# Kernel tuning notes

Hardware: AMD Instinct MI355X
Metric: run time of the kernel (lower is better)

## Reference

```python
import jax, jax.numpy as jnp
import numpy as np

TEMP = 0.7
ALPHA_ADV = 1.0
BETA_BAND = 0.5
BAND_L = 0.05
BAND_H = 0.2
W_HEUR = 0.5
W_LEAR = 0.5


def setup_inputs() -> dict:
    key = jax.random.key(0)
    ks = jax.random.split(key, 6)
    B, Sn, C, H, W = 2, 5, 64, 192, 192
    hid = 64
    return {
        "S": jax.random.normal(ks[0], (B, C, H, W), jnp.float32),
        "T": jax.random.normal(ks[1], (B, Sn, C, H, W), jnp.float32),
        "adapt_w": jax.random.normal(ks[2], (Sn, C, C), jnp.float32) / np.sqrt(C).astype(np.float32),
        "adapt_b": jnp.zeros((Sn, C), jnp.float32),
        "r_w1": jax.random.normal(ks[3], (hid, Sn * C * 3), jnp.float32) * 0.05,
        "r_b1": jnp.zeros((hid,), jnp.float32),
        "r_w2": jax.random.normal(ks[4], (Sn, hid), jnp.float32) * 0.05,
        "r_b2": jnp.zeros((Sn,), jnp.float32),
        "ema_mu": jnp.zeros((1, Sn, C, 1, 1), jnp.float32),
        "ema_sigma": jnp.ones((1, Sn, C, 1, 1), jnp.float32),
        "ema_proxy": jnp.zeros((1, Sn, 1, 1, 1), jnp.float32),
    }


def reference(S, T, adapt_w, adapt_b, r_w1, r_b1, r_w2, r_b2, ema_mu, ema_sigma, ema_proxy):
    B, Sn, C, H, W = T.shape
    bias = adapt_b[None, :, :, None, None]
    # per-sweep 1x1 conv == per-sweep channel matmul
    T_adapt = jnp.einsum('sdc,bschw->bsdhw', adapt_w, T) + bias          # [B,S,C,H,W]
    S_rep = jnp.einsum('sdc,bchw->bsdhw', adapt_w, S) + bias             # [B,S,C,H,W]
    Tz = (T_adapt - ema_mu) / ema_sigma
    Sz = (S_rep - ema_mu) / ema_sigma
    delta = Tz - Sz
    proxy = jnp.mean(delta * delta, axis=2, keepdims=True)               # [B,S,1,H,W]
    cur = jnp.mean(proxy, axis=(0, 3, 4), keepdims=True)                 # [1,S,1,1,1]
    # heuristic score (gamma_ucb = 0 -> no UCB term)
    impr = jax.lax.stop_gradient(ema_proxy - cur)
    adv = impr - jnp.mean(impr, axis=1, keepdims=True)
    below = jnp.maximum(BAND_L - cur, 0.0)
    above = jnp.maximum(cur - BAND_H, 0.0)
    band = -(below * below + above * above)
    score = ALPHA_ADV * adv + BETA_BAND * band                           # [1,S,1,1,1]
    score_heur = jnp.broadcast_to(score, proxy.shape)[:, :, 0]           # [B,S,H,W]
    # learned router: concat along channel of each sweep then 1x1 MLP
    x = jnp.concatenate([Sz, Tz, delta], axis=2).reshape(B, Sn * 3 * C, H, W)
    h = jax.nn.relu(jnp.einsum('oi,bihw->bohw', r_w1, x) + r_b1[None, :, None, None])
    score_learn = jnp.einsum('oi,bihw->bohw', r_w2, h) + r_b2[None, :, None, None]
    logits = W_HEUR * score_heur + W_LEAR * score_learn                  # [B,S,H,W]
    weights = jax.nn.softmax(logits / TEMP, axis=1)                      # soft gating over sweeps
    return weights
```

## Files before the change

### kernel.cpp

```cpp
#include <hip/hip_runtime.h>
#include <math.h>

#define HWSZ 36864
#define NBLK4 1152

typedef short bf16x8 __attribute__((ext_vector_type(8)));
typedef float f32x16 __attribute__((ext_vector_type(16)));
typedef unsigned int u32x4 __attribute__((ext_vector_type(4)));

__device__ __forceinline__ unsigned short f2bf(float x) {
    unsigned u = __float_as_uint(x);
    return (unsigned short)((u + 0x7fffu + ((u >> 16) & 1u)) >> 16);
}

__device__ __forceinline__ void block_sync_lds() {
    __builtin_amdgcn_sched_barrier(0);
    asm volatile("s_waitcnt lgkmcnt(0)" ::: "memory");
    __builtin_amdgcn_s_barrier();
    __builtin_amdgcn_sched_barrier(0);
}

__global__ void pre_all(const float* __restrict__ rw1, const float* __restrict__ rb1,
                        const float* __restrict__ aw, const float* __restrict__ ab,
                        const float* __restrict__ mu, const float* __restrict__ sg,
                        unsigned short* __restrict__ AfragW,
                        unsigned short* __restrict__ AfragMS2, float* __restrict__ c1) {
    int i = blockIdx.x * 256 + threadIdx.x;
    if (i < 40960) {
        int s = i / 8192, rem = i % 8192;
        int r = rem / 2048, rem2 = rem % 2048;
        int t = rem2 / 512, q = rem2 % 512;
        int l = q >> 3, e = q & 7;
        int R = 32 * r + (l & 31);
        int k = 16 * t + 8 * (l >> 5) + e;
        float v;
        if (R < 64) {
            v = aw[s * 4096 + R * 64 + k] / sg[s * 64 + R];
        } else {
            int o = R - 64;
            const float* wp = rw1 + o * 960 + s * 192;
            const float* A  = aw + s * 4096 + k;
            const float* G  = sg + s * 64;
            float sum = 0.f;
            #pragma unroll 8
            for (int d = 0; d < 64; ++d)
                sum = fmaf(wp[64 + d] + wp[128 + d], A[d * 64] / G[d], sum);
            v = sum;
        }
        AfragW[i] = f2bf(v);
    } else if (i < 45056) {
        int j = i - 40960;
        int r = j / 2048, rem2 = j % 2048;
        int t = rem2 / 512, q = rem2 % 512;
        int l = q >> 3, e = q & 7;
        int o = 32 * r + (l & 31);
        int k = 16 * t + 8 * (l >> 5) + e;
        float sum = 0.f;
        for (int s = 0; s < 5; ++s) {
            const float* wp = rw1 + o * 960 + s * 192;
            const float* A  = aw + s * 4096 + k;
            const float* G  = sg + s * 64;
            #pragma unroll 8
            for (int d = 0; d < 64; ++d)
                sum = fmaf(wp[d] - wp[128 + d], A[d * 64] / G[d], sum);
        }
        AfragMS2[j] = f2bf(sum);
    } else if (i < 45120) {
        int o = i - 45056;
        float sum = rb1[o];
        for (int s = 0; s < 5; ++s) {
            const float* wp = rw1 + o * 960 + s * 192;
            #pragma unroll 8
            for (int d = 0; d < 64; ++d) {
                int sd = s * 64 + d;
                sum = fmaf(wp[d] + wp[64 + d], (ab[sd] - mu[sd]) / sg[sd], sum);
            }
        }
        c1[o] = sum;
    }
}

__global__ __launch_bounds__(256, 4) void fused_main(
        const float* __restrict__ S, const float* __restrict__ T,
        const unsigned short* __restrict__ AfragW, const unsigned short* __restrict__ AfragMS2,
        const float* __restrict__ c1, const float* __restrict__ rw2, const float* __restrict__ rb2,
        float* __restrict__ slearn, float* __restrict__ partial) {
    __shared__ __align__(16) unsigned short sTile[4096];
    __shared__ __align__(16) unsigned short tbuf[2][4096];
    __shared__ float hpart[2][5][64];
    __shared__ float wred[5][2];
    __shared__ float w2s[320];
    __shared__ float c1s[64];
    __shared__ float rb2s[8];

    const int tid = threadIdx.x, lane = tid & 63, w = tid >> 6;
    const int hi = lane >> 5, pxm = lane & 31;
    const int blk = blockIdx.x;
    const int b = blk / 576;
    const int pix0 = (blk % 576) * 64;

    const int o8 = tid >> 5, q = tid & 31;
    const int skt = o8 >> 1, shh = o8 & 1;
    const float* Sp = S + ((size_t)(b * 64 + 8 * o8)) * HWSZ + pix0 + 2 * q;
    const float* Tp = T + ((size_t)(b * 5 * 64 + 8 * o8)) * HWSZ + pix0 + 2 * q;

    float2 R[8];
    #pragma unroll
    for (int j = 0; j < 8; ++j) R[j] = *(const float2*)(Sp + (size_t)j * HWSZ);

    for (int i = tid; i < 320; i += 256) w2s[i] = rw2[i];
    if (tid < 64) c1s[tid] = c1[tid];
    if (tid < 5)  rb2s[tid] = rb2[tid];

    auto packWrite = [&](unsigned short* dst) {
        #pragma unroll
        for (int h2 = 0; h2 < 2; ++h2) {
            int px = 2 * q + h2;
            int ct = px >> 5, slot = (px & 31) ^ ct;
            u32x4 v;
            #pragma unroll
            for (int jj = 0; jj < 4; ++jj) {
                float a = h2 ? R[2 * jj].y : R[2 * jj].x;
                float c = h2 ? R[2 * jj + 1].y : R[2 * jj + 1].x;
                v[jj] = (unsigned)f2bf(a) | ((unsigned)f2bf(c) << 16);
            }
            *(u32x4*)&dst[(((ct * 4 + skt) * 64) + shh * 32 + slot) * 8] = v;
        }
    };

    packWrite(sTile);

    #pragma unroll
    for (int j = 0; j < 8; ++j) R[j] = *(const float2*)(Tp + (size_t)j * HWSZ);

    const bf16x8* afw = (const bf16x8*)AfragW + lane;
    bf16x8 fr0[4], fr1[4];
    #pragma unroll
    for (int kt = 0; kt < 4; ++kt) fr0[kt] = afw[((0 * 4 + w) * 4 + kt) * 64];
    bf16x8 ms2f[4];
    if (w >= 2) {
        const bf16x8* am = (const bf16x8*)AfragMS2 + lane;
        #pragma unroll
        for (int kt = 0; kt < 4; ++kt) ms2f[kt] = am[((w - 2) * 4 + kt) * 64];
    }

    block_sync_lds();

    auto ldsB = [&](const unsigned short* buf, int ct, int kt) -> bf16x8 {
        return *(const bf16x8*)&buf[(((ct * 4 + kt) * 64) + hi * 32 + (pxm ^ ct)) * 8];
    };

    f32x16 acc0, acc1;
    #pragma unroll
    for (int i = 0; i < 16; ++i) { acc0[i] = 0.f; acc1[i] = 0.f; }

    if (w >= 2) {
        #pragma unroll
        for (int kt = 0; kt < 4; ++kt) {
            acc0 = __builtin_amdgcn_mfma_f32_32x32x16_bf16(ms2f[kt], ldsB(sTile, 0, kt), acc0, 0, 0, 0);
            acc1 = __builtin_amdgcn_mfma_f32_32x32x16_bf16(ms2f[kt], ldsB(sTile, 1, kt), acc1, 0, 0, 0);
        }
    }

    packWrite(tbuf[0]);
    #pragma unroll
    for (int j = 0; j < 8; ++j) R[j] = *(const float2*)(Tp + (size_t)(64 + j) * HWSZ);

    block_sync_lds();

    #pragma unroll
    for (int s = 0; s < 5; ++s) {
        const unsigned short* cur = tbuf[s & 1];
        unsigned short* nxt = tbuf[(s + 1) & 1];
        bf16x8* fcur = (s & 1) ? fr1 : fr0;
        bf16x8* fnxt = (s & 1) ? fr0 : fr1;
        if (s < 4) {
            #pragma unroll
            for (int kt = 0; kt < 4; ++kt) fnxt[kt] = afw[(((s + 1) * 4 + w) * 4 + kt) * 64];
        }
        if (w < 2) {
            #pragma unroll
            for (int i = 0; i < 16; ++i) { acc0[i] = 0.f; acc1[i] = 0.f; }
            #pragma unroll
            for (int kt = 0; kt < 4; ++kt) {
                acc0 = __builtin_amdgcn_mfma_f32_32x32x16_bf16(fcur[kt], ldsB(sTile, 0, kt), acc0, 0, 0, 0);
                acc1 = __builtin_amdgcn_mfma_f32_32x32x16_bf16(fcur[kt], ldsB(sTile, 1, kt), acc1, 0, 0, 0);
            }
            #pragma unroll
            for (int i = 0; i < 16; ++i) { acc0[i] = -acc0[i]; acc1[i] = -acc1[i]; }
            #pragma unroll
            for (int kt = 0; kt < 4; ++kt) {
                acc0 = __builtin_amdgcn_mfma_f32_32x32x16_bf16(fcur[kt], ldsB(cur, 0, kt), acc0, 0, 0, 0);
                acc1 = __builtin_amdgcn_mfma_f32_32x32x16_bf16(fcur[kt], ldsB(cur, 1, kt), acc1, 0, 0, 0);
            }
            float sq = 0.f;
            #pragma unroll
            for (int i = 0; i < 16; ++i) { sq = fmaf(acc0[i], acc0[i], sq); sq = fmaf(acc1[i], acc1[i], sq); }
            #pragma unroll
            for (int m = 1; m < 64; m <<= 1) sq += __shfl_xor(sq, m, 64);
            if (lane == 0) wred[s][w] = sq;
        } else {
            #pragma unroll
            for (int kt = 0; kt < 4; ++kt) {
                acc0 = __builtin_amdgcn_mfma_f32_32x32x16_bf16(fcur[kt], ldsB(cur, 0, kt), acc0, 0, 0, 0);
                acc1 = __builtin_amdgcn_mfma_f32_32x32x16_bf16(fcur[kt], ldsB(cur, 1, kt), acc1, 0, 0, 0);
            }
        }
        if (s < 4) {
            packWrite(nxt);
            if (s < 3) {
                #pragma unroll
                for (int j = 0; j < 8; ++j)
                    R[j] = *(const float2*)(Tp + (size_t)((s + 2) * 64 + j) * HWSZ);
            }
        }
        block_sync_lds();
    }

    if (w >= 2) {
        #pragma unroll
        for (int i = 0; i < 16; ++i) {
            int row = (i & 3) + 8 * (i >> 2) + 4 * hi + 32 * (w - 2);
            acc0[i] = fmaxf(acc0[i] + c1s[row], 0.f);
            acc1[i] = fmaxf(acc1[i] + c1s[row], 0.f);
        }
        #pragma unroll
        for (int sp = 0; sp < 5; ++sp) {
            float d0 = 0.f, d1 = 0.f;
            #pragma unroll
            for (int i = 0; i < 16; ++i) {
                int row = (i & 3) + 8 * (i >> 2) + 4 * hi + 32 * (w - 2);
                d0 = fmaf(w2s[sp * 64 + row], acc0[i], d0);
                d1 = fmaf(w2s[sp * 64 + row], acc1[i], d1);
            }
            d0 += __shfl_xor(d0, 32, 64);
            d1 += __shfl_xor(d1, 32, 64);
            if (hi == 0) { hpart[w - 2][sp][pxm] = d0; hpart[w - 2][sp][32 + pxm] = d1; }
        }
    }
    block_sync_lds();
    if (tid < 5) partial[blk * 5 + tid] = wred[tid][0] + wred[tid][1];
    for (int i = tid; i < 320; i += 256) {
        int sp = i >> 6, px = i & 63;
        slearn[((size_t)(b * 5 + sp)) * HWSZ + pix0 + px] =
            hpart[0][sp][px] + hpart[1][sp][px] + rb2s[sp];
    }
}

__global__ void score_kernel(const float* __restrict__ partial,
                             const float* __restrict__ ema_proxy,
                             float* __restrict__ scoreBuf) {
    __shared__ float red[256];
    __shared__ float cur[5];
    int tid = threadIdx.x;
    for (int s = 0; s < 5; ++s) {
        float sum = 0.f;
        for (int i = tid; i < NBLK4; i += 256) sum += partial[i * 5 + s];
        red[tid] = sum;
        __syncthreads();
        for (int off = 128; off > 0; off >>= 1) {
            if (tid < off) red[tid] += red[tid + off];
            __syncthreads();
        }
        if (tid == 0) cur[s] = red[0] * (1.0f / (64.0f * 2.0f * HWSZ));
        __syncthreads();
    }
    if (tid == 0) {
        float impr[5]; float m = 0.f;
        for (int s = 0; s < 5; ++s) { impr[s] = ema_proxy[s] - cur[s]; m += impr[s]; }
        m *= 0.2f;
        for (int s = 0; s < 5; ++s) {
            float adv = impr[s] - m;
            float c = cur[s];
            float below = fmaxf(0.05f - c, 0.f);
            float above = fmaxf(c - 0.2f, 0.f);
            float band = -(below * below + above * above);
            scoreBuf[s] = 1.0f * adv + 0.5f * band;
        }
    }
}

__global__ void softmax_kernel(const float* __restrict__ slearn,
                               const float* __restrict__ scoreBuf,
                               float* __restrict__ out) {
    int i = blockIdx.x * 256 + threadIdx.x;
    if (i >= 2 * HWSZ) return;
    int b = i / HWSZ, p = i % HWSZ;
    float l[5];
    float mx = -1e30f;
    #pragma unroll
    for (int s = 0; s < 5; ++s) {
        float v = (0.5f * scoreBuf[s] + 0.5f * slearn[((size_t)(b * 5 + s)) * HWSZ + p]) / 0.7f;
        l[s] = v;
        mx = fmaxf(mx, v);
    }
    float sum = 0.f;
    #pragma unroll
    for (int s = 0; s < 5; ++s) { l[s] = expf(l[s] - mx); sum += l[s]; }
    float inv = 1.0f / sum;
    #pragma unroll
    for (int s = 0; s < 5; ++s) out[((size_t)(b * 5 + s)) * HWSZ + p] = l[s] * inv;
}

extern "C" void kernel_launch(void* const* d_in, const int* in_sizes, int n_in,
                              void* d_out, int out_size, void* d_ws, size_t ws_size,
                              hipStream_t stream) {
    const float* S   = (const float*)d_in[0];
    const float* T   = (const float*)d_in[1];
    const float* aw  = (const float*)d_in[2];
    const float* ab  = (const float*)d_in[3];
    const float* rw1 = (const float*)d_in[4];
    const float* rb1 = (const float*)d_in[5];
    const float* rw2 = (const float*)d_in[6];
    const float* rb2 = (const float*)d_in[7];
    const float* mu  = (const float*)d_in[8];
    const float* sg  = (const float*)d_in[9];
    const float* ep  = (const float*)d_in[10];

    float* ws = (float*)d_ws;
    float* c1f      = ws;
    float* scoreBuf = ws + 64;
    float* partial  = ws + 72;
    unsigned short* AfragW   = (unsigned short*)(ws + 5832);
    unsigned short* AfragMS2 = (unsigned short*)(ws + 26312);
    float* slearn   = ws + 28360;
    float* out = (float*)d_out;

    pre_all<<<177, 256, 0, stream>>>(rw1, rb1, aw, ab, mu, sg, AfragW, AfragMS2, c1f);
    fused_main<<<NBLK4, 256, 0, stream>>>(S, T, AfragW, AfragMS2, c1f, rw2, rb2, slearn, partial);
    score_kernel<<<1, 256, 0, stream>>>(partial, ep, scoreBuf);
    softmax_kernel<<<288, 256, 0, stream>>>(slearn, scoreBuf, out);
}
```

Baseline: 56.11 us.

## Split fused kernel into bf16 transpose pass and register-fed MFMA GEMM

Adds an xpose kernel that reads S and T once, computes T−S, and writes bf16 tiles already laid out as MFMA B-operand fragments (X=T−S per sweep plus S). A new gemm_main then loads these fragments straight from global memory into registers, with no LDS staging. The algebra is refactored so the hidden layer uses a separate S-projection (AfragSp) plus per-sweep delta terms. The extra global write and re-read of the bf16 intermediates (about 47 MB) costs bandwidth in exchange for simpler, better-pipelined GEMM loads. The old fused kernel remains as a fallback when the workspace is too small.

```diff
diff --git a/kernel.cpp b/kernel.cpp
--- a/kernel.cpp
+++ b/kernel.cpp
@@ -2,7 +2,8 @@
 #include <math.h>
 
 #define HWSZ 36864
-#define NBLK4 1152
+#define NTILE64 576
+#define NBLK 1152
 
 typedef short bf16x8 __attribute__((ext_vector_type(8)));
 typedef float f32x16 __attribute__((ext_vector_type(16)));
@@ -24,7 +25,8 @@
                         const float* __restrict__ aw, const float* __restrict__ ab,
                         const float* __restrict__ mu, const float* __restrict__ sg,
                         unsigned short* __restrict__ AfragW,
-                        unsigned short* __restrict__ AfragMS2, float* __restrict__ c1) {
+                        unsigned short* __restrict__ AfragMS2,
+                        unsigned short* __restrict__ AfragSp, float* __restrict__ c1) {
     int i = blockIdx.x * 256 + threadIdx.x;
     if (i < 40960) {
         int s = i / 8192, rem = i % 8192;
@@ -48,8 +50,9 @@
             v = sum;
         }
         AfragW[i] = f2bf(v);
-    } else if (i < 45056) {
-        int j = i - 40960;
+    } else if (i < 49152) {
+        int j = (i - 40960) & 4095;
+        bool isSp = (i >= 45056);
         int r = j / 2048, rem2 = j % 2048;
         int t = rem2 / 512, q = rem2 % 512;
         int l = q >> 3, e = q & 7;
@@ -60,13 +63,19 @@
             const float* wp = rw1 + o * 960 + s * 192;
             const float* A  = aw + s * 4096 + k;
             const float* G  = sg + s * 64;
-            #pragma unroll 8
-            for (int d = 0; d < 64; ++d)
-                sum = fmaf(wp[d] - wp[128 + d], A[d * 64] / G[d], sum);
-        }
-        AfragMS2[j] = f2bf(sum);
-    } else if (i < 45120) {
-        int o = i - 45056;
+            if (isSp) {
+                #pragma unroll 8
+                for (int d = 0; d < 64; ++d)
+                    sum = fmaf(wp[d] + wp[64 + d], A[d * 64] / G[d], sum);
+            } else {
+                #pragma unroll 8
+                for (int d = 0; d < 64; ++d)
+                    sum = fmaf(wp[d] - wp[128 + d], A[d * 64] / G[d], sum);
+            }
+        }
+        if (isSp) AfragSp[j] = f2bf(sum); else AfragMS2[j] = f2bf(sum);
+    } else if (i < 49216) {
+        int o = i - 49152;
         float sum = rb1[o];
         for (int s = 0; s < 5; ++s) {
             const float* wp = rw1 + o * 960 + s * 192;
@@ -80,7 +89,198 @@
     }
 }
 
-__global__ __launch_bounds__(256, 4) void fused_main(
+__global__ __launch_bounds__(256) void xpose(
+        const float* __restrict__ S, const float* __restrict__ T,
+        unsigned short* __restrict__ Xf, unsigned short* __restrict__ Sf) {
+    __shared__ __align__(16) unsigned short tile[16384];
+    const int tid = threadIdx.x, w = tid >> 6, lane = tid & 63;
+    const int bid = blockIdx.x;
+    const int sidx = bid % 5;
+    const int chunk = (bid / 5) % 144;
+    const int b = bid / 720;
+    const int px0 = chunk * 256;
+
+    const float* Sb = S + ((size_t)(b * 64) + w * 16) * HWSZ + px0 + lane * 4;
+    const float* Tb = T + (((size_t)(b * 5) + sidx) * 64 + w * 16) * HWSZ + px0 + lane * 4;
+
+    float4 sv[16], tv[16];
+    #pragma unroll
+    for (int k = 0; k < 16; ++k) sv[k] = *(const float4*)(Sb + (size_t)k * HWSZ);
+    #pragma unroll
+    for (int k = 0; k < 16; ++k) tv[k] = *(const float4*)(Tb + (size_t)k * HWSZ);
+
+    auto stage = [&](bool isX) {
+        #pragma unroll
+        for (int k = 0; k < 16; ++k) {
+            int hh = k >> 3, e = k & 7;
+            #pragma unroll
+            for (int pi = 0; pi < 4; ++pi) {
+                int px = lane * 4 + pi;
+                int tl = px >> 6, px64 = px & 63, ct = px64 >> 5, pxm = px64 & 31;
+                float v = isX ? (((const float*)&tv[k])[pi] - ((const float*)&sv[k])[pi])
+                              : ((const float*)&sv[k])[pi];
+                tile[tl * 4096 + ((ct * 4 + w) * 64 + hh * 32 + pxm) * 8 + e] = f2bf(v);
+            }
+        }
+    };
+    auto writeout = [&](unsigned short* dstbase, size_t tstride_u16) {
+        int tl = tid >> 6;
+        const u32x4* src = (const u32x4*)&tile[tl * 4096];
+        u32x4* dst = (u32x4*)(dstbase + (size_t)tl * tstride_u16);
+        #pragma unroll
+        for (int k2 = 0; k2 < 8; ++k2) dst[k2 * 64 + lane] = src[k2 * 64 + lane];
+    };
+
+    stage(true);
+    block_sync_lds();
+    {
+        int t0 = chunk * 4;
+        unsigned short* xb = Xf + (((size_t)(b * NTILE64 + t0)) * 5 + sidx) * 4096;
+        writeout(xb, 5 * 4096);
+    }
+    if (sidx == 0) {
+        block_sync_lds();
+        stage(false);
+        block_sync_lds();
+        int t0 = chunk * 4;
+        unsigned short* sb = Sf + (size_t)(b * NTILE64 + t0) * 4096;
+        writeout(sb, 4096);
+    }
+}
+
+__global__ __launch_bounds__(256, 3) void gemm_main(
+        const unsigned short* __restrict__ Xf, const unsigned short* __restrict__ Sf,
+        const unsigned short* __restrict__ AfragW, const unsigned short* __restrict__ AfragSp,
+        const float* __restrict__ c1, const float* __restrict__ rw2, const float* __restrict__ rb2,
+        float* __restrict__ slearn, float* __restrict__ partial) {
+    __shared__ float wred[5][2];
+    __shared__ float hpart[2][5][64];
+    __shared__ float w2s[320];
+    __shared__ float c1s[64];
+    __shared__ float rb2s[8];
+
+    const int tid = threadIdx.x, lane = tid & 63, w = tid >> 6;
+    const int hi = lane >> 5, pxm = lane & 31;
+    const int bid = blockIdx.x;
+    const int b = bid / NTILE64, t = bid % NTILE64;
+    const int pix0 = t * 64;
+
+    for (int i = tid; i < 320; i += 256) w2s[i] = rw2[i];
+    if (tid < 64) c1s[tid] = c1[tid];
+    if (tid < 5)  rb2s[tid] = rb2[tid];
+
+    const bf16x8* xt = (const bf16x8*)(Xf + ((size_t)(b * NTILE64 + t) * 5) * 4096);
+    const bf16x8* st = (const bf16x8*)(Sf + (size_t)(b * NTILE64 + t) * 4096);
+    const bf16x8* afw = (const bf16x8*)AfragW + lane;
+
+    if (w < 2) {
+        bf16x8 bXc[8], bXn[8], fDc[4], fDn[4];
+        #pragma unroll
+        for (int i = 0; i < 8; ++i) bXc[i] = xt[i * 64 + lane];
+        #pragma unroll
+        for (int kt = 0; kt < 4; ++kt) fDc[kt] = afw[((0 * 4 + w) * 4 + kt) * 64];
+        #pragma unroll
+        for (int s = 0; s < 5; ++s) {
+            if (s < 4) {
+                #pragma unroll
+                for (int i = 0; i < 8; ++i) bXn[i] = xt[(size_t)(s + 1) * 512 + i * 64 + lane];
+                #pragma unroll
+                for (int kt = 0; kt < 4; ++kt) fDn[kt] = afw[(((s + 1) * 4 + w) * 4 + kt) * 64];
+            }
+            f32x16 d0, d1;
+            #pragma unroll
+            for (int i = 0; i < 16; ++i) { d0[i] = 0.f; d1[i] = 0.f; }
+            #pragma unroll
+            for (int kt = 0; kt < 4; ++kt) {
+                d0 = __builtin_amdgcn_mfma_f32_32x32x16_bf16(fDc[kt], bXc[kt],     d0, 0, 0, 0);
+                d1 = __builtin_amdgcn_mfma_f32_32x32x16_bf16(fDc[kt], bXc[4 + kt], d1, 0, 0, 0);
+            }
+            float sq = 0.f;
+            #pragma unroll
+            for (int i = 0; i < 16; ++i) { sq = fmaf(d0[i], d0[i], sq); sq = fmaf(d1[i], d1[i], sq); }
+            #pragma unroll
+            for (int m = 1; m < 64; m <<= 1) sq += __shfl_xor(sq, m, 64);
+            if (lane == 0) wred[s][w] = sq;
+            if (s < 4) {
+                #pragma unroll
+                for (int i = 0; i < 8; ++i) bXc[i] = bXn[i];
+                #pragma unroll
+                for (int kt = 0; kt < 4; ++kt) fDc[kt] = fDn[kt];
+            }
+        }
+    } else {
+        const int r = w - 2;
+        f32x16 h0, h1;
+        #pragma unroll
+        for (int i = 0; i < 16; ++i) { h0[i] = 0.f; h1[i] = 0.f; }
+        {
+            bf16x8 bS[8], msf[4];
+            #pragma unroll
+            for (int i = 0; i < 8; ++i) bS[i] = st[i * 64 + lane];
+            const bf16x8* asp = (const bf16x8*)AfragSp + lane;
+            #pragma unroll
+            for (int kt = 0; kt < 4; ++kt) msf[kt] = asp[(r * 4 + kt) * 64];
+            #pragma unroll
+            for (int kt = 0; kt < 4; ++kt) {
+                h0 = __builtin_amdgcn_mfma_f32_32x32x16_bf16(msf[kt], bS[kt],     h0, 0, 0, 0);
+                h1 = __builtin_amdgcn_mfma_f32_32x32x16_bf16(msf[kt], bS[4 + kt], h1, 0, 0, 0);
+            }
+        }
+        bf16x8 bXc[8], bXn[8], fMc[4], fMn[4];
+        #pragma unroll
+        for (int i = 0; i < 8; ++i) bXc[i] = xt[i * 64 + lane];
+        #pragma unroll
+        for (int kt = 0; kt < 4; ++kt) fMc[kt] = afw[((0 * 4 + 2 + r) * 4 + kt) * 64];
+        #pragma unroll
+        for (int s = 0; s < 5; ++s) {
+            if (s < 4) {
+                #pragma unroll
+                for (int i = 0; i < 8; ++i) bXn[i] = xt[(size_t)(s + 1) * 512 + i * 64 + lane];
+                #pragma unroll
+                for (int kt = 0; kt < 4; ++kt) fMn[kt] = afw[(((s + 1) * 4 + 2 + r) * 4 + kt) * 64];
+            }
+            #pragma unroll
+            for (int kt = 0; kt < 4; ++kt) {
+                h0 = __builtin_amdgcn_mfma_f32_32x32x16_bf16(fMc[kt], bXc[kt],     h0, 0, 0, 0);
+                h1 = __builtin_amdgcn_mfma_f32_32x32x16_bf16(fMc[kt], bXc[4 + kt], h1, 0, 0, 0);
+            }
+            if (s < 4) {
+                #pragma unroll
+                for (int i = 0; i < 8; ++i) bXc[i] = bXn[i];
+                #pragma unroll
+                for (int kt = 0; kt < 4; ++kt) fMc[kt] = fMn[kt];
+            }
+        }
+        #pragma unroll
+        for (int i = 0; i < 16; ++i) {
+            int row = (i & 3) + 8 * (i >> 2) + 4 * hi + 32 * r;
+            h0[i] = fmaxf(h0[i] + c1s[row], 0.f);
+            h1[i] = fmaxf(h1[i] + c1s[row], 0.f);
+        }
+        #pragma unroll
+        for (int sp = 0; sp < 5; ++sp) {
+            float d0 = 0.f, d1 = 0.f;
+            #pragma unroll
+            for (int i = 0; i < 16; ++i) {
+                int row = (i & 3) + 8 * (i >> 2) + 4 * hi + 32 * r;
+                d0 = fmaf(w2s[sp * 64 + row], h0[i], d0);
+                d1 = fmaf(w2s[sp * 64 + row], h1[i], d1);
+            }
+            d0 += __shfl_xor(d0, 32, 64);
+            d1 += __shfl_xor(d1, 32, 64);
+            if (hi == 0) { hpart[r][sp][pxm] = d0; hpart[r][sp][32 + pxm] = d1; }
+        }
+    }
+    block_sync_lds();
+    if (tid < 5) partial[bid * 5 + tid] = wred[tid][0] + wred[tid][1];
+    for (int i = tid; i < 320; i += 256) {
+        int sp = i >> 6, px = i & 63;
+        slearn[((size_t)(b * 5 + sp)) * HWSZ + pix0 + px] =
+            hpart[0][sp][px] + hpart[1][sp][px] + rb2s[sp];
+    }
+}
+
+__global__ __launch_bounds__(256, 4) void fused_fallback(
         const float* __restrict__ S, const float* __restrict__ T,
         const unsigned short* __restrict__ AfragW, const unsigned short* __restrict__ AfragMS2,
         const float* __restrict__ c1, const float* __restrict__ rw2, const float* __restrict__ rb2,
@@ -98,7 +298,6 @@
     const int blk = blockIdx.x;
     const int b = blk / 576;
     const int pix0 = (blk % 576) * 64;
-
     const int o8 = tid >> 5, q = tid & 31;
     const int skt = o8 >> 1, shh = o8 & 1;
     const float* Sp = S + ((size_t)(b * 64 + 8 * o8)) * HWSZ + pix0 + 2 * q;
@@ -107,7 +306,6 @@
     float2 R[8];
     #pragma unroll
     for (int j = 0; j < 8; ++j) R[j] = *(const float2*)(Sp + (size_t)j * HWSZ);
-
     for (int i = tid; i < 320; i += 256) w2s[i] = rw2[i];
     if (tid < 64) c1s[tid] = c1[tid];
     if (tid < 5)  rb2s[tid] = rb2[tid];
@@ -127,9 +325,7 @@
             *(u32x4*)&dst[(((ct * 4 + skt) * 64) + shh * 32 + slot) * 8] = v;
         }
     };
-
     packWrite(sTile);
-
     #pragma unroll
     for (int j = 0; j < 8; ++j) R[j] = *(const float2*)(Tp + (size_t)j * HWSZ);
 
@@ -143,7 +339,6 @@
         #pragma unroll
         for (int kt = 0; kt < 4; ++kt) ms2f[kt] = am[((w - 2) * 4 + kt) * 64];
     }
-
     block_sync_lds();
 
     auto ldsB = [&](const unsigned short* buf, int ct, int kt) -> bf16x8 {
@@ -153,7 +348,6 @@
     f32x16 acc0, acc1;
     #pragma unroll
     for (int i = 0; i < 16; ++i) { acc0[i] = 0.f; acc1[i] = 0.f; }
-
     if (w >= 2) {
         #pragma unroll
         for (int kt = 0; kt < 4; ++kt) {
@@ -161,11 +355,9 @@
             acc1 = __builtin_amdgcn_mfma_f32_32x32x16_bf16(ms2f[kt], ldsB(sTile, 1, kt), acc1, 0, 0, 0);
         }
     }
-
     packWrite(tbuf[0]);
     #pragma unroll
     for (int j = 0; j < 8; ++j) R[j] = *(const float2*)(Tp + (size_t)(64 + j) * HWSZ);
-
     block_sync_lds();
 
     #pragma unroll
@@ -255,7 +447,7 @@
     int tid = threadIdx.x;
     for (int s = 0; s < 5; ++s) {
         float sum = 0.f;
-        for (int i = tid; i < NBLK4; i += 256) sum += partial[i * 5 + s];
+        for (int i = tid; i < NBLK; i += 256) sum += partial[i * 5 + s];
         red[tid] = sum;
         __syncthreads();
         for (int off = 128; off > 0; off >>= 1) {
@@ -322,12 +514,21 @@
     float* scoreBuf = ws + 64;
     float* partial  = ws + 72;
     unsigned short* AfragW   = (unsigned short*)(ws + 5832);
-    unsigned short* AfragMS2 = (unsigned short*)(ws + 26312);
-    float* slearn   = ws + 28360;
+    unsigned short* AfragSp  = (unsigned short*)(ws + 26312);
+    unsigned short* AfragMS2 = (unsigned short*)(ws + 28360);
+    float* slearn   = ws + 30408;
+    unsigned short* Xf = (unsigned short*)(ws + 399048);
+    unsigned short* Sf = (unsigned short*)(ws + 12195528);
+    const size_t NEED_BYTES = 14554824UL * 4UL;
     float* out = (float*)d_out;
 
-    pre_all<<<177, 256, 0, stream>>>(rw1, rb1, aw, ab, mu, sg, AfragW, AfragMS2, c1f);
-    fused_main<<<NBLK4, 256, 0, stream>>>(S, T, AfragW, AfragMS2, c1f, rw2, rb2, slearn, partial);
+    pre_all<<<193, 256, 0, stream>>>(rw1, rb1, aw, ab, mu, sg, AfragW, AfragMS2, AfragSp, c1f);
+    if (ws_size >= NEED_BYTES) {
+        xpose<<<1440, 256, 0, stream>>>(S, T, Xf, Sf);
+        gemm_main<<<NBLK, 256, 0, stream>>>(Xf, Sf, AfragW, AfragSp, c1f, rw2, rb2, slearn, partial);
+    } else {
+        fused_fallback<<<NBLK, 256, 0, stream>>>(S, T, AfragW, AfragMS2, c1f, rw2, rb2, slearn, partial);
+    }
     score_kernel<<<1, 256, 0, stream>>>(partial, ep, scoreBuf);
     softmax_kernel<<<288, 256, 0, stream>>>(slearn, scoreBuf, out);
 }
```

After: 89.78 us. 60.0% more time.
